# Kernel tuning notes

Hardware: AMD Instinct MI355X
Metric: run time of the kernel (lower is better)

The kernel has to match this reference:

```python
import jax, jax.numpy as jnp
import numpy as np

N = 20000
E = 320000
IN_C = 256
HID = 64
OUT_C = 64
NUM_LAYERS = 3
HEADS = 8


def setup_inputs() -> dict:
    key = jax.random.key(0)
    ks = jax.random.split(key, 12)
    s_in = 1.0 / np.sqrt(IN_C)
    s_h = 1.0 / np.sqrt(HID)
    inp = {
        "x": jax.random.normal(ks[0], (N, IN_C), dtype=jnp.float32),
        "edge_index": jax.random.randint(ks[1], (2, E), 0, N, dtype=jnp.int64),
        "lin1_w": jax.random.uniform(ks[2], (IN_C, HID), jnp.float32, -s_in, s_in),
        "lin1_b": jnp.zeros((HID,), jnp.float32),
        "wq": jax.random.uniform(ks[3], (NUM_LAYERS, HID, HID), jnp.float32, -s_h, s_h),
        "bq": jnp.zeros((NUM_LAYERS, HID), jnp.float32),
        "wk": jax.random.uniform(ks[4], (NUM_LAYERS, HID, HID), jnp.float32, -s_h, s_h),
        "bk": jnp.zeros((NUM_LAYERS, HID), jnp.float32),
        "wv": jax.random.uniform(ks[5], (NUM_LAYERS, HID, HID), jnp.float32, -s_h, s_h),
        "bv": jnp.zeros((NUM_LAYERS, HID), jnp.float32),
        "lin2_w": jax.random.uniform(ks[6], (HID, OUT_C), jnp.float32, -s_h, s_h),
        "lin2_b": jnp.zeros((OUT_C,), jnp.float32),
    }
    return inp


def reference(x, edge_index, lin1_w, lin1_b, wq, bq, wk, bk, wv, bv, lin2_w, lin2_b):
    n = x.shape[0]
    C = lin1_w.shape[1]
    d = C // HEADS  # per-head dim
    inv_sqrt_d = 1.0 / (d ** 0.5)

    # gcn_norm with self-loops (symmetric normalization, edge weights = 1)
    loop = jnp.arange(n, dtype=edge_index.dtype)
    row = jnp.concatenate([edge_index[0], loop])  # source j
    col = jnp.concatenate([edge_index[1], loop])  # target i
    deg = jax.ops.segment_sum(jnp.ones_like(col, dtype=x.dtype), col, num_segments=n)
    dinv = jnp.where(deg > 0, deg ** -0.5, 0.0)
    norm = dinv[row] * dinv[col]  # [E+N]

    # input projection (dropout inactive in eval mode)
    h = jax.nn.relu(x @ lin1_w + lin1_b)
    x_all = h[:, None, :]  # [N, 1, C] growing history

    for l in range(NUM_LAYERS):
        t = x_all.shape[1]
        # node-level projections (linear commutes with gather)
        q = x_all[:, -1] @ wq[l] + bq[l]                      # [N, C]
        k = jnp.einsum("ntc,cd->ntd", x_all, wk[l]) + bk[l]   # [N, t, C]
        v = jnp.einsum("ntc,cd->ntd", x_all, wv[l]) + bv[l]   # [N, t, C]
        # per-edge multi-head attention of target's latest repr over source history
        Qe = q[col].reshape(-1, HEADS, d)                      # [E', H, d]
        Ke = k[row].reshape(-1, t, HEADS, d)                   # [E', t, H, d]
        Ve = v[row].reshape(-1, t, HEADS, d)
        scores = jnp.einsum("ehd,ethd->eht", Qe, Ke) * inv_sqrt_d
        attn = jax.nn.softmax(scores, axis=-1)                 # [E', H, t]
        msg = jnp.einsum("eht,ethd->ehd", attn, Ve).reshape(-1, C)
        msg = msg * norm[:, None]
        out = jax.ops.segment_sum(msg, col, num_segments=n)    # sum aggregation
        out = jax.nn.relu(out)
        x_all = jnp.concatenate([x_all, out[:, None, :]], axis=1)

    logits = x_all[:, -1] @ lin2_w + lin2_b
    return jax.nn.log_softmax(logits, axis=1)
```

## Files before the change

### kernel.cpp

```cpp
#include <hip/hip_runtime.h>
#include <math.h>

#define HID 64
#define HEADS 8
#define NUM_LAYERS 3

typedef __attribute__((ext_vector_type(8))) short bf16x8;
typedef __attribute__((ext_vector_type(4))) float f32x4;

__device__ __forceinline__ unsigned short f2bf(float f) {
    union { float f; unsigned int u; } cv; cv.f = f;
    unsigned int u = cv.u;
    unsigned int r = (u + 0x7FFFu + ((u >> 16) & 1u)) >> 16;
    return (unsigned short)r;
}
__device__ __forceinline__ float bflo(unsigned int u) {
    union { unsigned int u; float f; } cv; cv.u = u << 16; return cv.f;
}
__device__ __forceinline__ float bfhi(unsigned int u) {
    union { unsigned int u; float f; } cv; cv.u = u & 0xFFFF0000u; return cv.f;
}
__device__ __forceinline__ unsigned relu_pk(unsigned u) {
    unsigned m = ((u & 0x8000u) ? 0u : 0xFFFFu) |
                 ((u & 0x80000000u) ? 0u : 0xFFFF0000u);
    return u & m;
}

__global__ void k_count(const int* __restrict__ col, int* __restrict__ counts, int E) {
    int e = blockIdx.x * blockDim.x + threadIdx.x;
    if (e < E) atomicAdd(&counts[col[e]], 1);
}

__global__ __launch_bounds__(1024) void k_scan(const int* __restrict__ counts,
                                               int* __restrict__ start,
                                               float* __restrict__ dinv, int n) {
    __shared__ int wsum[16];
    int tid = threadIdx.x;
    int lane = tid & 63, wv = tid >> 6;
    int ipt = (n + 1023) >> 10;
    int c0 = tid * ipt;
    int c1 = min(n, c0 + ipt);
    int s = 0;
    for (int i = c0; i < c1; ++i) s += counts[i];
    int x = s;
#pragma unroll
    for (int off = 1; off < 64; off <<= 1) {
        int y = __shfl_up(x, off);
        if (lane >= off) x += y;
    }
    if (lane == 63) wsum[wv] = x;
    __syncthreads();
    if (wv == 0 && lane < 16) {
        int t2 = wsum[lane];
#pragma unroll
        for (int off = 1; off < 16; off <<= 1) {
            int y = __shfl_up(t2, off);
            if (lane >= off) t2 += y;
        }
        wsum[lane] = t2;
    }
    __syncthreads();
    int waveoff = (wv > 0) ? wsum[wv - 1] : 0;
    int run = waveoff + x - s;
    for (int i = c0; i < c1; ++i) {
        int v = counts[i];
        start[i] = run;
        dinv[i] = rsqrtf((float)(v + 1));
        run += v;
    }
    if (tid == 0) start[n] = wsum[15];
}

__global__ void k_scatter(const int* __restrict__ ei, const int* __restrict__ start,
                          int* __restrict__ fill, int* __restrict__ ebuf, int E) {
    int e = blockIdx.x * blockDim.x + threadIdx.x;
    if (e >= E) return;
    int r = ei[e], c = ei[E + e];
    int pos = start[c] + atomicAdd(&fill[c], 1);
    ebuf[pos] = r;
}

#define ALD 72

__device__ __forceinline__ void stage_w_bf16(unsigned short* Wt,
                                             const float* __restrict__ w, int tid) {
    for (int idx = tid; idx < 1024; idx += 256) {
        int k = idx >> 4, n4 = (idx & 15) * 4;
        float4 wv = *(const float4*)&w[k * 64 + n4];
        Wt[(n4 + 0) * ALD + k] = f2bf(wv.x);
        Wt[(n4 + 1) * ALD + k] = f2bf(wv.y);
        Wt[(n4 + 2) * ALD + k] = f2bf(wv.z);
        Wt[(n4 + 3) * ALD + k] = f2bf(wv.w);
    }
}

__device__ __forceinline__ void mfma_step(const unsigned short* Alds,
                                          const unsigned short* Wt,
                                          int tid, f32x4 acc[4]) {
    int lane = tid & 63;
    int m0 = (tid >> 6) * 16;
    int c16 = lane & 15, quad = lane >> 4;
    const unsigned short* ar = &Alds[(m0 + c16) * ALD + quad * 8];
    bf16x8 a0 = *(const bf16x8*)ar;
    bf16x8 a1 = *(const bf16x8*)(ar + 32);
#pragma unroll
    for (int nt = 0; nt < 4; ++nt) {
        const unsigned short* br = &Wt[(nt * 16 + c16) * ALD + quad * 8];
        bf16x8 b0 = *(const bf16x8*)br;
        bf16x8 b1 = *(const bf16x8*)(br + 32);
        acc[nt] = __builtin_amdgcn_mfma_f32_16x16x32_bf16(a0, b0, acc[nt], 0, 0, 0);
        acc[nt] = __builtin_amdgcn_mfma_f32_16x16x32_bf16(a1, b1, acc[nt], 0, 0, 0);
    }
}

__global__ __launch_bounds__(256, 4) void k_lin1(
    const float* __restrict__ x, const float* __restrict__ w,
    const float* __restrict__ b, const float* __restrict__ wv0,
    const float* __restrict__ bv0, unsigned short* __restrict__ h,
    unsigned short* __restrict__ kv, int n) {
    __shared__ __align__(16) unsigned short Alds[64 * ALD];
    __shared__ __align__(16) unsigned short Wt[64 * ALD];
    int tid = threadIdx.x;
    int node0 = blockIdx.x * 64;
    f32x4 acc[4];
#pragma unroll
    for (int nt = 0; nt < 4; ++nt) acc[nt] = (f32x4){0.f, 0.f, 0.f, 0.f};

    for (int kc = 0; kc < 256; kc += 64) {
        __syncthreads();
        stage_w_bf16(Wt, w + kc * 64, tid);
        for (int idx = tid; idx < 1024; idx += 256) {
            int r = idx >> 4, c4 = (idx & 15) * 4;
            int node = node0 + r;
            float4 v = make_float4(0.f, 0.f, 0.f, 0.f);
            if (node < n) v = *(const float4*)&x[(size_t)node * 256 + kc + c4];
            Alds[r * ALD + c4 + 0] = f2bf(v.x);
            Alds[r * ALD + c4 + 1] = f2bf(v.y);
            Alds[r * ALD + c4 + 2] = f2bf(v.z);
            Alds[r * ALD + c4 + 3] = f2bf(v.w);
        }
        __syncthreads();
        mfma_step(Alds, Wt, tid, acc);
    }
    int lane = tid & 63;
    int m0 = (tid >> 6) * 16, c16 = lane & 15, quad = lane >> 4;
    float bias[4];
#pragma unroll
    for (int nt = 0; nt < 4; ++nt) bias[nt] = b[nt * 16 + c16];

    __syncthreads();
    stage_w_bf16(Wt, wv0, tid);
#pragma unroll
    for (int i = 0; i < 4; ++i) {
        int row = m0 + quad * 4 + i;
        int node = node0 + row;
#pragma unroll
        for (int nt = 0; nt < 4; ++nt) {
            unsigned short hb = f2bf(fmaxf(acc[nt][i] + bias[nt], 0.f));
            Alds[row * ALD + nt * 16 + c16] = hb;
            if (node < n) h[(size_t)node * 64 + nt * 16 + c16] = hb;
        }
    }
    __syncthreads();
    f32x4 acc2[4];
#pragma unroll
    for (int nt = 0; nt < 4; ++nt) acc2[nt] = (f32x4){0.f, 0.f, 0.f, 0.f};
    mfma_step(Alds, Wt, tid, acc2);
    float bias2[4];
#pragma unroll
    for (int nt = 0; nt < 4; ++nt) bias2[nt] = bv0[nt * 16 + c16];
#pragma unroll
    for (int i = 0; i < 4; ++i) {
        int node = node0 + m0 + quad * 4 + i;
        if (node < n) {
#pragma unroll
            for (int nt = 0; nt < 4; ++nt)
                kv[(size_t)node * 64 + nt * 16 + c16] = f2bf(acc2[nt][i] + bias2[nt]);
        }
    }
}

__global__ __launch_bounds__(256, 4) void k_qkv(
    const unsigned short* __restrict__ xsbase,
    const float* __restrict__ wq, const float* __restrict__ bq,
    const float* __restrict__ wk, const float* __restrict__ bk,
    const float* __restrict__ wv, const float* __restrict__ bv,
    float* __restrict__ q, unsigned short* __restrict__ kv,
    int n, int layer, int t, int kv_stride) {
    int job = blockIdx.y;
    const unsigned short* src; const float* w; const float* b; bool relu_in;
    int kv_off = 0;
    if (job == 0) {
        src = xsbase + (size_t)layer * n * 64;
        w = wq + layer * 4096; b = bq + layer * 64;
        relu_in = (layer >= 1);
    } else if (job <= t) {
        int s = job - 1;
        src = xsbase + (size_t)s * n * 64;
        w = wk + layer * 4096; b = bk + layer * 64;
        kv_off = s * 128;
        relu_in = (s >= 1);
    } else {
        int s = job - t - 1;
        src = xsbase + (size_t)s * n * 64;
        w = wv + layer * 4096; b = bv + layer * 64;
        kv_off = s * 128 + 64;
        relu_in = (s >= 1);
    }
    __shared__ __align__(16) unsigned short Alds[64 * ALD];
    __shared__ __align__(16) unsigned short Wt[64 * ALD];
    int tid = threadIdx.x;
    int node0 = blockIdx.x * 64;
    stage_w_bf16(Wt, w, tid);
    for (int idx = tid; idx < 512; idx += 256) {
        int r = idx >> 3, seg = idx & 7;
        int node = node0 + r;
        uint4 u = make_uint4(0u, 0u, 0u, 0u);
        if (node < n) u = *(const uint4*)&src[(size_t)node * 64 + seg * 8];
        if (relu_in) {
            u.x = relu_pk(u.x); u.y = relu_pk(u.y);
            u.z = relu_pk(u.z); u.w = relu_pk(u.w);
        }
        *(uint4*)&Alds[r * ALD + seg * 8] = u;
    }
    __syncthreads();
    f32x4 acc[4];
#pragma unroll
    for (int nt = 0; nt < 4; ++nt) acc[nt] = (f32x4){0.f, 0.f, 0.f, 0.f};
    mfma_step(Alds, Wt, tid, acc);

    int lane = tid & 63;
    int m0 = (tid >> 6) * 16, c16 = lane & 15, quad = lane >> 4;
    float bias[4];
#pragma unroll
    for (int nt = 0; nt < 4; ++nt) bias[nt] = b[nt * 16 + c16];
    if (job == 0) {
#pragma unroll
        for (int i = 0; i < 4; ++i) {
            int node = node0 + m0 + quad * 4 + i;
            if (node < n) {
#pragma unroll
                for (int nt = 0; nt < 4; ++nt)
                    q[(size_t)node * 64 + nt * 16 + c16] = acc[nt][i] + bias[nt];
            }
        }
    } else {
#pragma unroll
        for (int i = 0; i < 4; ++i) {
            int node = node0 + m0 + quad * 4 + i;
            if (node < n) {
#pragma unroll
                for (int nt = 0; nt < 4; ++nt)
                    kv[(size_t)node * kv_stride + kv_off + nt * 16 + c16] =
                        f2bf(acc[nt][i] + bias[nt]);
            }
        }
    }
}

template <int T>
__global__ __launch_bounds__(256) void k_attn_g(
    const int* __restrict__ start, const int* __restrict__ ebuf,
    const float* __restrict__ dinv, const float* __restrict__ q,
    const unsigned short* __restrict__ kv, unsigned short* __restrict__ outp, int n) {
    const int KVS = (T == 1) ? 64 : T * 128;
    int node = (int)((blockIdx.x * (size_t)blockDim.x + threadIdx.x) >> 6);
    int lane = threadIdx.x & 63;
    if (node >= n) return;
    int g = lane >> 3;
    int cb = (lane & 7) * 8;
    const float isd = 0.35355339059327373f;

    float qv[8];
    if (T > 1) {
        float4 q0 = *(const float4*)&q[(size_t)node * 64 + cb];
        float4 q1 = *(const float4*)&q[(size_t)node * 64 + cb + 4];
        qv[0] = q0.x; qv[1] = q0.y; qv[2] = q0.z; qv[3] = q0.w;
        qv[4] = q1.x; qv[5] = q1.y; qv[6] = q1.z; qv[7] = q1.w;
    }
    float dc = dinv[node];
    int s0 = start[node];
    int cnt = start[node + 1] - s0 + 1;

    float acc[8];
#pragma unroll
    for (int k = 0; k < 8; ++k) acc[k] = 0.f;

    for (int base = 0; base < cnt; base += 8) {
        int idx = base + g;
        bool valid = idx < cnt;
        int r = node;
        if (valid && idx > 0) r = ebuf[s0 + idx - 1];
        float dr = valid ? dinv[r] : 0.f;
        const unsigned short* rkv = kv + (size_t)r * KVS;

        float sc[T];
        float wgt;
        if (T > 1) {
            float m = -1e30f;
#pragma unroll
            for (int s = 0; s < T; ++s) {
                uint4 ku = *(const uint4*)&rkv[s * 128 + cb];
                float p = qv[0] * bflo(ku.x) + qv[1] * bfhi(ku.x)
                        + qv[2] * bflo(ku.y) + qv[3] * bfhi(ku.y)
                        + qv[4] * bflo(ku.z) + qv[5] * bfhi(ku.z)
                        + qv[6] * bflo(ku.w) + qv[7] * bfhi(ku.w);
                p *= isd;
                sc[s] = p;
                m = fmaxf(m, p);
            }
            float denom = 0.f;
#pragma unroll
            for (int s = 0; s < T; ++s) { sc[s] = __expf(sc[s] - m); denom += sc[s]; }
            wgt = dr / denom;
        } else {
            sc[0] = 1.f;
            wgt = dr;
        }

        float mg[8];
#pragma unroll
        for (int k = 0; k < 8; ++k) mg[k] = 0.f;
#pragma unroll
        for (int s = 0; s < T; ++s) {
            uint4 vu = *(const uint4*)&rkv[((T == 1) ? 0 : s * 128 + 64) + cb];
            float wv_ = sc[s];
            mg[0] += wv_ * bflo(vu.x); mg[1] += wv_ * bfhi(vu.x);
            mg[2] += wv_ * bflo(vu.y); mg[3] += wv_ * bfhi(vu.y);
            mg[4] += wv_ * bflo(vu.z); mg[5] += wv_ * bfhi(vu.z);
            mg[6] += wv_ * bflo(vu.w); mg[7] += wv_ * bfhi(vu.w);
        }
#pragma unroll
        for (int k = 0; k < 8; ++k) acc[k] += wgt * mg[k];
    }

#pragma unroll
    for (int off = 8; off < 64; off <<= 1) {
#pragma unroll
        for (int k = 0; k < 8; ++k) acc[k] += __shfl_xor(acc[k], off);
    }
    if (g == 0) {
        ushort4 o0, o1;
        o0.x = f2bf(acc[0] * dc); o0.y = f2bf(acc[1] * dc);
        o0.z = f2bf(acc[2] * dc); o0.w = f2bf(acc[3] * dc);
        o1.x = f2bf(acc[4] * dc); o1.y = f2bf(acc[5] * dc);
        o1.z = f2bf(acc[6] * dc); o1.w = f2bf(acc[7] * dc);
        *(ushort4*)&outp[(size_t)node * 64 + cb] = o0;
        *(ushort4*)&outp[(size_t)node * 64 + cb + 4] = o1;
    }
}

__global__ __launch_bounds__(256) void k_attn3f(
    const int* __restrict__ start, const int* __restrict__ ebuf,
    const float* __restrict__ dinv, const float* __restrict__ q,
    const unsigned short* __restrict__ kv,
    const float* __restrict__ w2, const float* __restrict__ b2,
    float* __restrict__ outp, int n) {
    const int T = 3, KVS = 384;
    int node = (int)((blockIdx.x * (size_t)blockDim.x + threadIdx.x) >> 6);
    int lane = threadIdx.x & 63;
    if (node >= n) return;
    int g = lane >> 3;
    int cb = (lane & 7) * 8;
    const float isd = 0.35355339059327373f;

    float qv[8];
    {
        float4 q0 = *(const float4*)&q[(size_t)node * 64 + cb];
        float4 q1 = *(const float4*)&q[(size_t)node * 64 + cb + 4];
        qv[0] = q0.x; qv[1] = q0.y; qv[2] = q0.z; qv[3] = q0.w;
        qv[4] = q1.x; qv[5] = q1.y; qv[6] = q1.z; qv[7] = q1.w;
    }
    float dc = dinv[node];
    int s0 = start[node];
    int cnt = start[node + 1] - s0 + 1;

    float acc[8];
#pragma unroll
    for (int k = 0; k < 8; ++k) acc[k] = 0.f;

    for (int base = 0; base < cnt; base += 8) {
        int idx = base + g;
        bool valid = idx < cnt;
        int r = node;
        if (valid && idx > 0) r = ebuf[s0 + idx - 1];
        float dr = valid ? dinv[r] : 0.f;
        const unsigned short* rkv = kv + (size_t)r * KVS;

        float sc[T];
        float m = -1e30f;
#pragma unroll
        for (int s = 0; s < T; ++s) {
            uint4 ku = *(const uint4*)&rkv[s * 128 + cb];
            float p = qv[0] * bflo(ku.x) + qv[1] * bfhi(ku.x)
                    + qv[2] * bflo(ku.y) + qv[3] * bfhi(ku.y)
                    + qv[4] * bflo(ku.z) + qv[5] * bfhi(ku.z)
                    + qv[6] * bflo(ku.w) + qv[7] * bfhi(ku.w);
            p *= isd;
            sc[s] = p;
            m = fmaxf(m, p);
        }
        float denom = 0.f;
#pragma unroll
        for (int s = 0; s < T; ++s) { sc[s] = __expf(sc[s] - m); denom += sc[s]; }
        float wgt = dr / denom;

        float mg[8];
#pragma unroll
        for (int k = 0; k < 8; ++k) mg[k] = 0.f;
#pragma unroll
        for (int s = 0; s < T; ++s) {
            uint4 vu = *(const uint4*)&rkv[s * 128 + 64 + cb];
            float wv_ = sc[s];
            mg[0] += wv_ * bflo(vu.x); mg[1] += wv_ * bfhi(vu.x);
            mg[2] += wv_ * bflo(vu.y); mg[3] += wv_ * bfhi(vu.y);
            mg[4] += wv_ * bflo(vu.z); mg[5] += wv_ * bfhi(vu.z);
            mg[6] += wv_ * bflo(vu.w); mg[7] += wv_ * bfhi(vu.w);
        }
#pragma unroll
        for (int k = 0; k < 8; ++k) acc[k] += wgt * mg[k];
    }

#pragma unroll
    for (int off = 8; off < 64; off <<= 1) {
#pragma unroll
        for (int k = 0; k < 8; ++k) acc[k] += __shfl_xor(acc[k], off);
    }
    float lg = b2[lane];
#pragma unroll
    for (int c = 0; c < 64; ++c) {
        float xc = fmaxf(__shfl(acc[c & 7], c >> 3) * dc, 0.f);
        lg += xc * w2[c * 64 + lane];
    }
    float mx = lg;
#pragma unroll
    for (int off = 1; off < 64; off <<= 1) mx = fmaxf(mx, __shfl_xor(mx, off));
    float e = __expf(lg - mx);
    float ssum = e;
#pragma unroll
    for (int off = 1; off < 64; off <<= 1) ssum += __shfl_xor(ssum, off);
    outp[(size_t)node * 64 + lane] = lg - mx - __logf(ssum);
}

extern "C" void kernel_launch(void* const* d_in, const int* in_sizes, int n_in,
                              void* d_out, int out_size, void* d_ws, size_t ws_size,
                              hipStream_t stream) {
    const float* x  = (const float*)d_in[0];
    const int*   ei = (const int*)d_in[1];
    const float* w1 = (const float*)d_in[2];
    const float* b1 = (const float*)d_in[3];
    const float* wq = (const float*)d_in[4];
    const float* bq = (const float*)d_in[5];
    const float* wk = (const float*)d_in[6];
    const float* bk = (const float*)d_in[7];
    const float* wv = (const float*)d_in[8];
    const float* bv = (const float*)d_in[9];
    const float* w2 = (const float*)d_in[10];
    const float* b2 = (const float*)d_in[11];
    float* outp = (float*)d_out;

    int n = in_sizes[0] / 256;
    int E = in_sizes[1] / 2;

    float* ws = (float*)d_ws;
    size_t off = 0;
    float* dinv = ws + off; off += (size_t)n;
    float* q    = ws + off; off += (size_t)n * 64;
    unsigned short* xsU = (unsigned short*)(ws + off); off += (size_t)n * 96;
    unsigned short* kvU = (unsigned short*)(ws + off); off += (size_t)n * 192;
    int* wsI    = (int*)(ws + off);
    int* counts = wsI;
    int* fill   = wsI + n;
    int* startA = wsI + 2 * n;
    int* ebuf   = wsI + 3 * n + 1;

    hipMemsetAsync(counts, 0, 2 * (size_t)n * sizeof(int), stream);
    k_count<<<(E + 255) / 256, 256, 0, stream>>>(ei + E, counts, E);
    k_scan<<<1, 1024, 0, stream>>>(counts, startA, dinv, n);
    k_scatter<<<(E + 255) / 256, 256, 0, stream>>>(ei, startA, fill, ebuf, E);

    k_lin1<<<(n + 63) / 64, 256, 0, stream>>>(x, w1, b1, wv, bv, xsU, kvU, n);

    int attn_grid = (int)(((size_t)n * 64 + 255) / 256);

    k_attn_g<1><<<attn_grid, 256, 0, stream>>>(startA, ebuf, dinv, q, kvU,
                                               xsU + (size_t)n * 64, n);
    {
        dim3 grid((n + 63) / 64, 5);
        k_qkv<<<grid, 256, 0, stream>>>(xsU, wq, bq, wk, bk, wv, bv,
                                        q, kvU, n, 1, 2, 256);
        k_attn_g<2><<<attn_grid, 256, 0, stream>>>(startA, ebuf, dinv, q, kvU,
                                                   xsU + (size_t)n * 128, n);
    }
    {
        dim3 grid((n + 63) / 64, 7);
        k_qkv<<<grid, 256, 0, stream>>>(xsU, wq, bq, wk, bk, wv, bv,
                                        q, kvU, n, 2, 3, 384);
        k_attn3f<<<attn_grid, 256, 0, stream>>>(startA, ebuf, dinv, q, kvU,
                                                w2, b2, outp, n);
    }
}
```

Before: 265.6 us.

## Fuse whole pipeline into one cooperative persistent kernel with grid syncs

Replaces the sequence of separate launches (memset, count, scan, scatter, lin1, three attention layers and qkv projections) with one cooperative persistent kernel that separates phases with grid.sync. It also overlaps independent work inside phases: the degree count runs alongside lin1, and the layer-1/2 K/V projections of the lin1 output run alongside the scan. KV buffers are split per layer so these projections can be computed early. The aim is to remove launch gaps and tail idle time, at the cost of grid-wide barriers, a single block doing the scan, and fewer resident waves for the attention phases; the old launch path is kept as a fallback if the cooperative launch fails.

```diff
diff --git a/kernel.cpp b/kernel.cpp
--- a/kernel.cpp
+++ b/kernel.cpp
@@ -1,9 +1,13 @@
 #include <hip/hip_runtime.h>
+#include <hip/hip_cooperative_groups.h>
 #include <math.h>
+
+namespace cg = cooperative_groups;
 
 #define HID 64
 #define HEADS 8
 #define NUM_LAYERS 3
+#define ALD 72
 
 typedef __attribute__((ext_vector_type(8))) short bf16x8;
 typedef __attribute__((ext_vector_type(4))) float f32x4;
@@ -25,62 +29,6 @@
                  ((u & 0x80000000u) ? 0u : 0xFFFF0000u);
     return u & m;
 }
-
-__global__ void k_count(const int* __restrict__ col, int* __restrict__ counts, int E) {
-    int e = blockIdx.x * blockDim.x + threadIdx.x;
-    if (e < E) atomicAdd(&counts[col[e]], 1);
-}
-
-__global__ __launch_bounds__(1024) void k_scan(const int* __restrict__ counts,
-                                               int* __restrict__ start,
-                                               float* __restrict__ dinv, int n) {
-    __shared__ int wsum[16];
-    int tid = threadIdx.x;
-    int lane = tid & 63, wv = tid >> 6;
-    int ipt = (n + 1023) >> 10;
-    int c0 = tid * ipt;
-    int c1 = min(n, c0 + ipt);
-    int s = 0;
-    for (int i = c0; i < c1; ++i) s += counts[i];
-    int x = s;
-#pragma unroll
-    for (int off = 1; off < 64; off <<= 1) {
-        int y = __shfl_up(x, off);
-        if (lane >= off) x += y;
-    }
-    if (lane == 63) wsum[wv] = x;
-    __syncthreads();
-    if (wv == 0 && lane < 16) {
-        int t2 = wsum[lane];
-#pragma unroll
-        for (int off = 1; off < 16; off <<= 1) {
-            int y = __shfl_up(t2, off);
-            if (lane >= off) t2 += y;
-        }
-        wsum[lane] = t2;
-    }
-    __syncthreads();
-    int waveoff = (wv > 0) ? wsum[wv - 1] : 0;
-    int run = waveoff + x - s;
-    for (int i = c0; i < c1; ++i) {
-        int v = counts[i];
-        start[i] = run;
-        dinv[i] = rsqrtf((float)(v + 1));
-        run += v;
-    }
-    if (tid == 0) start[n] = wsum[15];
-}
-
-__global__ void k_scatter(const int* __restrict__ ei, const int* __restrict__ start,
-                          int* __restrict__ fill, int* __restrict__ ebuf, int E) {
-    int e = blockIdx.x * blockDim.x + threadIdx.x;
-    if (e >= E) return;
-    int r = ei[e], c = ei[E + e];
-    int pos = start[c] + atomicAdd(&fill[c], 1);
-    ebuf[pos] = r;
-}
-
-#define ALD 72
 
 __device__ __forceinline__ void stage_w_bf16(unsigned short* Wt,
                                              const float* __restrict__ w, int tid) {
@@ -113,15 +61,64 @@
     }
 }
 
-__global__ __launch_bounds__(256, 4) void k_lin1(
+__device__ __forceinline__ void qkv_tile_body(
+    const unsigned short* __restrict__ src, const float* __restrict__ w,
+    const float* __restrict__ b, float* __restrict__ qd,
+    unsigned short* __restrict__ kvdst, int kv_stride, int kv_off, bool relu_in,
+    int node0, int n, int tid, unsigned short* Alds, unsigned short* Wt) {
+    stage_w_bf16(Wt, w, tid);
+    for (int idx = tid; idx < 512; idx += 256) {
+        int r = idx >> 3, seg = idx & 7;
+        int node = node0 + r;
+        uint4 u = make_uint4(0u, 0u, 0u, 0u);
+        if (node < n) u = *(const uint4*)&src[(size_t)node * 64 + seg * 8];
+        if (relu_in) {
+            u.x = relu_pk(u.x); u.y = relu_pk(u.y);
+            u.z = relu_pk(u.z); u.w = relu_pk(u.w);
+        }
+        *(uint4*)&Alds[r * ALD + seg * 8] = u;
+    }
+    __syncthreads();
+    f32x4 acc[4];
+#pragma unroll
+    for (int nt = 0; nt < 4; ++nt) acc[nt] = (f32x4){0.f, 0.f, 0.f, 0.f};
+    mfma_step(Alds, Wt, tid, acc);
+
+    int lane = tid & 63;
+    int m0 = (tid >> 6) * 16, c16 = lane & 15, quad = lane >> 4;
+    float bias[4];
+#pragma unroll
+    for (int nt = 0; nt < 4; ++nt) bias[nt] = b[nt * 16 + c16];
+    if (qd) {
+#pragma unroll
+        for (int i = 0; i < 4; ++i) {
+            int node = node0 + m0 + quad * 4 + i;
+            if (node < n) {
+#pragma unroll
+                for (int nt = 0; nt < 4; ++nt)
+                    qd[(size_t)node * 64 + nt * 16 + c16] = acc[nt][i] + bias[nt];
+            }
+        }
+    } else {
+#pragma unroll
+        for (int i = 0; i < 4; ++i) {
+            int node = node0 + m0 + quad * 4 + i;
+            if (node < n) {
+#pragma unroll
+                for (int nt = 0; nt < 4; ++nt)
+                    kvdst[(size_t)node * kv_stride + kv_off + nt * 16 + c16] =
+                        f2bf(acc[nt][i] + bias[nt]);
+            }
+        }
+    }
+}
+
+__device__ __forceinline__ void lin1_tile_body(
     const float* __restrict__ x, const float* __restrict__ w,
     const float* __restrict__ b, const float* __restrict__ wv0,
     const float* __restrict__ bv0, unsigned short* __restrict__ h,
-    unsigned short* __restrict__ kv, int n) {
-    __shared__ __align__(16) unsigned short Alds[64 * ALD];
-    __shared__ __align__(16) unsigned short Wt[64 * ALD];
-    int tid = threadIdx.x;
-    int node0 = blockIdx.x * 64;
+    unsigned short* __restrict__ kv, int n, int node0, int tid,
+    unsigned short* Alds, unsigned short* Wt) {
     f32x4 acc[4];
 #pragma unroll
     for (int nt = 0; nt < 4; ++nt) acc[nt] = (f32x4){0.f, 0.f, 0.f, 0.f};
@@ -180,6 +177,396 @@
     }
 }
 
+__device__ __forceinline__ void scan256_body(const int* __restrict__ counts,
+                                             int* __restrict__ start,
+                                             float* __restrict__ dinv, int n,
+                                             int tid, int* sscan) {
+    int lane = tid & 63, wvi = tid >> 6;
+    int ipt = (n + 255) >> 8;
+    int c0 = tid * ipt;
+    int c1 = min(n, c0 + ipt);
+    int s = 0;
+    for (int i = c0; i < c1; ++i) s += counts[i];
+    int x = s;
+#pragma unroll
+    for (int off = 1; off < 64; off <<= 1) {
+        int y = __shfl_up(x, off);
+        if (lane >= off) x += y;
+    }
+    if (lane == 63) sscan[wvi] = x;
+    __syncthreads();
+    if (tid == 0) {
+        int r = 0;
+#pragma unroll
+        for (int i = 0; i < 4; ++i) { int t = sscan[i]; sscan[i + 4] = r; r += t; }
+        start[n] = r;
+    }
+    __syncthreads();
+    int run = sscan[wvi + 4] + (x - s);
+    for (int i = c0; i < c1; ++i) {
+        int v = counts[i];
+        start[i] = run;
+        dinv[i] = rsqrtf((float)(v + 1));
+        run += v;
+    }
+}
+
+template <int T>
+__device__ __forceinline__ void attn_body(
+    int node, int lane, const int* __restrict__ start, const int* __restrict__ ebuf,
+    const float* __restrict__ dinv, const float* __restrict__ q,
+    const unsigned short* __restrict__ kv, unsigned short* __restrict__ outp) {
+    const int KVS = (T == 1) ? 64 : T * 128;
+    int g = lane >> 3;
+    int cb = (lane & 7) * 8;
+    const float isd = 0.35355339059327373f;
+
+    float qv[8];
+    if (T > 1) {
+        float4 q0 = *(const float4*)&q[(size_t)node * 64 + cb];
+        float4 q1 = *(const float4*)&q[(size_t)node * 64 + cb + 4];
+        qv[0] = q0.x; qv[1] = q0.y; qv[2] = q0.z; qv[3] = q0.w;
+        qv[4] = q1.x; qv[5] = q1.y; qv[6] = q1.z; qv[7] = q1.w;
+    }
+    float dc = dinv[node];
+    int s0 = start[node];
+    int cnt = start[node + 1] - s0 + 1;
+
+    float acc[8];
+#pragma unroll
+    for (int k = 0; k < 8; ++k) acc[k] = 0.f;
+
+    for (int base = 0; base < cnt; base += 8) {
+        int idx = base + g;
+        bool valid = idx < cnt;
+        int r = node;
+        if (valid && idx > 0) r = ebuf[s0 + idx - 1];
+        float dr = valid ? dinv[r] : 0.f;
+        const unsigned short* rkv = kv + (size_t)r * KVS;
+
+        float sc[T];
+        float wgt;
+        if (T > 1) {
+            float m = -1e30f;
+#pragma unroll
+            for (int s = 0; s < T; ++s) {
+                uint4 ku = *(const uint4*)&rkv[s * 128 + cb];
+                float p = qv[0] * bflo(ku.x) + qv[1] * bfhi(ku.x)
+                        + qv[2] * bflo(ku.y) + qv[3] * bfhi(ku.y)
+                        + qv[4] * bflo(ku.z) + qv[5] * bfhi(ku.z)
+                        + qv[6] * bflo(ku.w) + qv[7] * bfhi(ku.w);
+                p *= isd;
+                sc[s] = p;
+                m = fmaxf(m, p);
+            }
+            float denom = 0.f;
+#pragma unroll
+            for (int s = 0; s < T; ++s) { sc[s] = __expf(sc[s] - m); denom += sc[s]; }
+            wgt = dr / denom;
+        } else {
+            sc[0] = 1.f;
+            wgt = dr;
+        }
+
+        float mg[8];
+#pragma unroll
+        for (int k = 0; k < 8; ++k) mg[k] = 0.f;
+#pragma unroll
+        for (int s = 0; s < T; ++s) {
+            uint4 vu = *(const uint4*)&rkv[((T == 1) ? 0 : s * 128 + 64) + cb];
+            float wv_ = sc[s];
+            mg[0] += wv_ * bflo(vu.x); mg[1] += wv_ * bfhi(vu.x);
+            mg[2] += wv_ * bflo(vu.y); mg[3] += wv_ * bfhi(vu.y);
+            mg[4] += wv_ * bflo(vu.z); mg[5] += wv_ * bfhi(vu.z);
+            mg[6] += wv_ * bflo(vu.w); mg[7] += wv_ * bfhi(vu.w);
+        }
+#pragma unroll
+        for (int k = 0; k < 8; ++k) acc[k] += wgt * mg[k];
+    }
+
+#pragma unroll
+    for (int off = 8; off < 64; off <<= 1) {
+#pragma unroll
+        for (int k = 0; k < 8; ++k) acc[k] += __shfl_xor(acc[k], off);
+    }
+    if (g == 0) {
+        ushort4 o0, o1;
+        o0.x = f2bf(acc[0] * dc); o0.y = f2bf(acc[1] * dc);
+        o0.z = f2bf(acc[2] * dc); o0.w = f2bf(acc[3] * dc);
+        o1.x = f2bf(acc[4] * dc); o1.y = f2bf(acc[5] * dc);
+        o1.z = f2bf(acc[6] * dc); o1.w = f2bf(acc[7] * dc);
+        *(ushort4*)&outp[(size_t)node * 64 + cb] = o0;
+        *(ushort4*)&outp[(size_t)node * 64 + cb + 4] = o1;
+    }
+}
+
+__device__ __forceinline__ void attn3_body(
+    int node, int lane, const int* __restrict__ start, const int* __restrict__ ebuf,
+    const float* __restrict__ dinv, const float* __restrict__ q,
+    const unsigned short* __restrict__ kv, const float* __restrict__ w2,
+    const float* __restrict__ b2, float* __restrict__ outp) {
+    const int T = 3, KVS = 384;
+    int g = lane >> 3;
+    int cb = (lane & 7) * 8;
+    const float isd = 0.35355339059327373f;
+
+    float qv[8];
+    {
+        float4 q0 = *(const float4*)&q[(size_t)node * 64 + cb];
+        float4 q1 = *(const float4*)&q[(size_t)node * 64 + cb + 4];
+        qv[0] = q0.x; qv[1] = q0.y; qv[2] = q0.z; qv[3] = q0.w;
+        qv[4] = q1.x; qv[5] = q1.y; qv[6] = q1.z; qv[7] = q1.w;
+    }
+    float dc = dinv[node];
+    int s0 = start[node];
+    int cnt = start[node + 1] - s0 + 1;
+
+    float acc[8];
+#pragma unroll
+    for (int k = 0; k < 8; ++k) acc[k] = 0.f;
+
+    for (int base = 0; base < cnt; base += 8) {
+        int idx = base + g;
+        bool valid = idx < cnt;
+        int r = node;
+        if (valid && idx > 0) r = ebuf[s0 + idx - 1];
+        float dr = valid ? dinv[r] : 0.f;
+        const unsigned short* rkv = kv + (size_t)r * KVS;
+
+        float sc[T];
+        float m = -1e30f;
+#pragma unroll
+        for (int s = 0; s < T; ++s) {
+            uint4 ku = *(const uint4*)&rkv[s * 128 + cb];
+            float p = qv[0] * bflo(ku.x) + qv[1] * bfhi(ku.x)
+                    + qv[2] * bflo(ku.y) + qv[3] * bfhi(ku.y)
+                    + qv[4] * bflo(ku.z) + qv[5] * bfhi(ku.z)
+                    + qv[6] * bflo(ku.w) + qv[7] * bfhi(ku.w);
+            p *= isd;
+            sc[s] = p;
+            m = fmaxf(m, p);
+        }
+        float denom = 0.f;
+#pragma unroll
+        for (int s = 0; s < T; ++s) { sc[s] = __expf(sc[s] - m); denom += sc[s]; }
+        float wgt = dr / denom;
+
+        float mg[8];
+#pragma unroll
+        for (int k = 0; k < 8; ++k) mg[k] = 0.f;
+#pragma unroll
+        for (int s = 0; s < T; ++s) {
+            uint4 vu = *(const uint4*)&rkv[s * 128 + 64 + cb];
+            float wv_ = sc[s];
+            mg[0] += wv_ * bflo(vu.x); mg[1] += wv_ * bfhi(vu.x);
+            mg[2] += wv_ * bflo(vu.y); mg[3] += wv_ * bfhi(vu.y);
+            mg[4] += wv_ * bflo(vu.z); mg[5] += wv_ * bfhi(vu.z);
+            mg[6] += wv_ * bflo(vu.w); mg[7] += wv_ * bfhi(vu.w);
+        }
+#pragma unroll
+        for (int k = 0; k < 8; ++k) acc[k] += wgt * mg[k];
+    }
+
+#pragma unroll
+    for (int off = 8; off < 64; off <<= 1) {
+#pragma unroll
+        for (int k = 0; k < 8; ++k) acc[k] += __shfl_xor(acc[k], off);
+    }
+    float lg = b2[lane];
+#pragma unroll
+    for (int c = 0; c < 64; ++c) {
+        float xc = fmaxf(__shfl(acc[c & 7], c >> 3) * dc, 0.f);
+        lg += xc * w2[c * 64 + lane];
+    }
+    float mx = lg;
+#pragma unroll
+    for (int off = 1; off < 64; off <<= 1) mx = fmaxf(mx, __shfl_xor(mx, off));
+    float e = __expf(lg - mx);
+    float ssum = e;
+#pragma unroll
+    for (int off = 1; off < 64; off <<= 1) ssum += __shfl_xor(ssum, off);
+    outp[(size_t)node * 64 + lane] = lg - mx - __logf(ssum);
+}
+
+__global__ __launch_bounds__(256, 4) void k_mega(
+    const float* __restrict__ x, const int* __restrict__ ei,
+    const float* __restrict__ w1, const float* __restrict__ b1,
+    const float* __restrict__ wq, const float* __restrict__ bq,
+    const float* __restrict__ wk, const float* __restrict__ bk,
+    const float* __restrict__ wv, const float* __restrict__ bv,
+    const float* __restrict__ w2, const float* __restrict__ b2,
+    float* __restrict__ outp, float* __restrict__ dinv, float* __restrict__ qbuf,
+    unsigned short* __restrict__ xsU, unsigned short* __restrict__ kv0,
+    unsigned short* __restrict__ kv1, unsigned short* __restrict__ kv2,
+    int* __restrict__ counts, int* __restrict__ fill, int* __restrict__ startA,
+    int* __restrict__ ebuf, int n, int E) {
+    cg::grid_group grid = cg::this_grid();
+    __shared__ __align__(16) unsigned short Alds[64 * ALD];
+    __shared__ __align__(16) unsigned short Wt[64 * ALD];
+    __shared__ int sscan[8];
+    const int tid = threadIdx.x;
+    const int bid = blockIdx.x;
+    const int NB = gridDim.x;
+    const int NT = (n + 63) >> 6;
+    const int lane = tid & 63;
+    const int wid = (bid << 2) + (tid >> 6);
+    const int nw = NB << 2;
+
+    for (int i = bid * 256 + tid; i < n; i += NB * 256) counts[i] = 0;
+    for (int i = bid * 256 + tid; i < n; i += NB * 256) fill[i] = 0;
+    grid.sync();
+
+    {
+        int l1b = (NB * 3) >> 2;
+        int L1B = NT < l1b ? NT : l1b;
+        if (L1B < 1) L1B = 1;
+        if (bid < L1B) {
+            for (int t = bid; t < NT; t += L1B)
+                lin1_tile_body(x, w1, b1, wv, bv, xsU, kv0, n, t << 6, tid, Alds, Wt);
+        } else {
+            int cb = bid - L1B, ncb = NB - L1B;
+            for (int e = cb * 256 + tid; e < E; e += ncb * 256)
+                atomicAdd(&counts[ei[E + e]], 1);
+        }
+    }
+    grid.sync();
+
+    if (bid == 0) {
+        scan256_body(counts, startA, dinv, n, tid, sscan);
+    } else {
+        for (int t = bid - 1; t < 4 * NT; t += NB - 1) {
+            int job = t / NT, tile = t - job * NT;
+            const float* w; const float* b; unsigned short* dst; int stride, koff;
+            if (job == 0)      { w = wk + 4096; b = bk + 64;  dst = kv1; stride = 256; koff = 0;  }
+            else if (job == 1) { w = wv + 4096; b = bv + 64;  dst = kv1; stride = 256; koff = 64; }
+            else if (job == 2) { w = wk + 8192; b = bk + 128; dst = kv2; stride = 384; koff = 0;  }
+            else               { w = wv + 8192; b = bv + 128; dst = kv2; stride = 384; koff = 64; }
+            __syncthreads();
+            qkv_tile_body(xsU, w, b, nullptr, dst, stride, koff, false,
+                          tile << 6, n, tid, Alds, Wt);
+        }
+    }
+    grid.sync();
+
+    for (int e = bid * 256 + tid; e < E; e += NB * 256) {
+        int r = ei[e], c = ei[E + e];
+        int pos = startA[c] + atomicAdd(&fill[c], 1);
+        ebuf[pos] = r;
+    }
+    grid.sync();
+
+    for (int node = wid; node < n; node += nw)
+        attn_body<1>(node, lane, startA, ebuf, dinv, qbuf, kv0, xsU + (size_t)n * 64);
+    grid.sync();
+
+    {
+        const unsigned short* xs1 = xsU + (size_t)n * 64;
+        for (int t = bid; t < 5 * NT; t += NB) {
+            int job = t / NT, tile = t - job * NT;
+            const float* w; const float* b;
+            float* qd = nullptr; unsigned short* dst = nullptr;
+            int stride = 0, koff = 0;
+            if (job == 0)      { w = wq + 4096; b = bq + 64; qd = qbuf; }
+            else if (job == 1) { w = wk + 4096; b = bk + 64;  dst = kv1; stride = 256; koff = 128; }
+            else if (job == 2) { w = wv + 4096; b = bv + 64;  dst = kv1; stride = 256; koff = 192; }
+            else if (job == 3) { w = wk + 8192; b = bk + 128; dst = kv2; stride = 384; koff = 128; }
+            else               { w = wv + 8192; b = bv + 128; dst = kv2; stride = 384; koff = 192; }
+            __syncthreads();
+            qkv_tile_body(xs1, w, b, qd, dst, stride, koff, true,
+                          tile << 6, n, tid, Alds, Wt);
+        }
+    }
+    grid.sync();
+
+    for (int node = wid; node < n; node += nw)
+        attn_body<2>(node, lane, startA, ebuf, dinv, qbuf, kv1, xsU + (size_t)n * 128);
+    grid.sync();
+
+    {
+        const unsigned short* xs2 = xsU + (size_t)n * 128;
+        for (int t = bid; t < 3 * NT; t += NB) {
+            int job = t / NT, tile = t - job * NT;
+            const float* w; const float* b;
+            float* qd = nullptr; unsigned short* dst = nullptr;
+            int stride = 0, koff = 0;
+            if (job == 0)      { w = wq + 8192; b = bq + 128; qd = qbuf; }
+            else if (job == 1) { w = wk + 8192; b = bk + 128; dst = kv2; stride = 384; koff = 256; }
+            else               { w = wv + 8192; b = bv + 128; dst = kv2; stride = 384; koff = 320; }
+            __syncthreads();
+            qkv_tile_body(xs2, w, b, qd, dst, stride, koff, true,
+                          tile << 6, n, tid, Alds, Wt);
+        }
+    }
+    grid.sync();
+
+    for (int node = wid; node < n; node += nw)
+        attn3_body(node, lane, startA, ebuf, dinv, qbuf, kv2, w2, b2, outp);
+}
+
+__global__ void k_count(const int* __restrict__ col, int* __restrict__ counts, int E) {
+    int e = blockIdx.x * blockDim.x + threadIdx.x;
+    if (e < E) atomicAdd(&counts[col[e]], 1);
+}
+
+__global__ __launch_bounds__(1024) void k_scan(const int* __restrict__ counts,
+                                               int* __restrict__ start,
+                                               float* __restrict__ dinv, int n) {
+    __shared__ int wsum[16];
+    int tid = threadIdx.x;
+    int lane = tid & 63, wvi = tid >> 6;
+    int ipt = (n + 1023) >> 10;
+    int c0 = tid * ipt;
+    int c1 = min(n, c0 + ipt);
+    int s = 0;
+    for (int i = c0; i < c1; ++i) s += counts[i];
+    int x = s;
+#pragma unroll
+    for (int off = 1; off < 64; off <<= 1) {
+        int y = __shfl_up(x, off);
+        if (lane >= off) x += y;
+    }
+    if (lane == 63) wsum[wvi] = x;
+    __syncthreads();
+    if (wvi == 0 && lane < 16) {
+        int t2 = wsum[lane];
+#pragma unroll
+        for (int off = 1; off < 16; off <<= 1) {
+            int y = __shfl_up(t2, off);
+            if (lane >= off) t2 += y;
+        }
+        wsum[lane] = t2;
+    }
+    __syncthreads();
+    int waveoff = (wvi > 0) ? wsum[wvi - 1] : 0;
+    int run = waveoff + x - s;
+    for (int i = c0; i < c1; ++i) {
+        int v = counts[i];
+        start[i] = run;
+        dinv[i] = rsqrtf((float)(v + 1));
+        run += v;
+    }
+    if (tid == 0) start[n] = wsum[15];
+}
+
+__global__ void k_scatter(const int* __restrict__ ei, const int* __restrict__ start,
+                          int* __restrict__ fill, int* __restrict__ ebuf, int E) {
+    int e = blockIdx.x * blockDim.x + threadIdx.x;
+    if (e >= E) return;
+    int r = ei[e], c = ei[E + e];
+    int pos = start[c] + atomicAdd(&fill[c], 1);
+    ebuf[pos] = r;
+}
+
+__global__ __launch_bounds__(256, 4) void k_lin1(
+    const float* __restrict__ x, const float* __restrict__ w,
+    const float* __restrict__ b, const float* __restrict__ wv0,
+    const float* __restrict__ bv0, unsigned short* __restrict__ h,
+    unsigned short* __restrict__ kv, int n) {
+    __shared__ __align__(16) unsigned short Alds[64 * ALD];
+    __shared__ __align__(16) unsigned short Wt[64 * ALD];
+    lin1_tile_body(x, w, b, wv0, bv0, h, kv, n, blockIdx.x * 64, threadIdx.x, Alds, Wt);
+}
+
 __global__ __launch_bounds__(256, 4) void k_qkv(
     const unsigned short* __restrict__ xsbase,
     const float* __restrict__ wq, const float* __restrict__ bq,
@@ -189,11 +576,11 @@
     int n, int layer, int t, int kv_stride) {
     int job = blockIdx.y;
     const unsigned short* src; const float* w; const float* b; bool relu_in;
-    int kv_off = 0;
+    int kv_off = 0; float* qd = nullptr;
     if (job == 0) {
         src = xsbase + (size_t)layer * n * 64;
         w = wq + layer * 4096; b = bq + layer * 64;
-        relu_in = (layer >= 1);
+        relu_in = (layer >= 1); qd = q;
     } else if (job <= t) {
         int s = job - 1;
         src = xsbase + (size_t)s * n * 64;
@@ -209,53 +596,8 @@
     }
     __shared__ __align__(16) unsigned short Alds[64 * ALD];
     __shared__ __align__(16) unsigned short Wt[64 * ALD];
-    int tid = threadIdx.x;
-    int node0 = blockIdx.x * 64;
-    stage_w_bf16(Wt, w, tid);
-    for (int idx = tid; idx < 512; idx += 256) {
-        int r = idx >> 3, seg = idx & 7;
-        int node = node0 + r;
-        uint4 u = make_uint4(0u, 0u, 0u, 0u);
-        if (node < n) u = *(const uint4*)&src[(size_t)node * 64 + seg * 8];
-        if (relu_in) {
-            u.x = relu_pk(u.x); u.y = relu_pk(u.y);
-            u.z = relu_pk(u.z); u.w = relu_pk(u.w);
-        }
-        *(uint4*)&Alds[r * ALD + seg * 8] = u;
-    }
-    __syncthreads();
-    f32x4 acc[4];
-#pragma unroll
-    for (int nt = 0; nt < 4; ++nt) acc[nt] = (f32x4){0.f, 0.f, 0.f, 0.f};
-    mfma_step(Alds, Wt, tid, acc);
-
-    int lane = tid & 63;
-    int m0 = (tid >> 6) * 16, c16 = lane & 15, quad = lane >> 4;
-    float bias[4];
-#pragma unroll
-    for (int nt = 0; nt < 4; ++nt) bias[nt] = b[nt * 16 + c16];
-    if (job == 0) {
-#pragma unroll
-        for (int i = 0; i < 4; ++i) {
-            int node = node0 + m0 + quad * 4 + i;
-            if (node < n) {
-#pragma unroll
-                for (int nt = 0; nt < 4; ++nt)
-                    q[(size_t)node * 64 + nt * 16 + c16] = acc[nt][i] + bias[nt];
-            }
-        }
-    } else {
-#pragma unroll
-        for (int i = 0; i < 4; ++i) {
-            int node = node0 + m0 + quad * 4 + i;
-            if (node < n) {
-#pragma unroll
-                for (int nt = 0; nt < 4; ++nt)
-                    kv[(size_t)node * kv_stride + kv_off + nt * 16 + c16] =
-                        f2bf(acc[nt][i] + bias[nt]);
-            }
-        }
-    }
+    qkv_tile_body(src, w, b, qd, kv, kv_stride, kv_off, relu_in,
+                  blockIdx.x * 64, n, threadIdx.x, Alds, Wt);
 }
 
 template <int T>
@@ -263,91 +605,9 @@
     const int* __restrict__ start, const int* __restrict__ ebuf,
     const float* __restrict__ dinv, const float* __restrict__ q,
     const unsigned short* __restrict__ kv, unsigned short* __restrict__ outp, int n) {
-    const int KVS = (T == 1) ? 64 : T * 128;
     int node = (int)((blockIdx.x * (size_t)blockDim.x + threadIdx.x) >> 6);
-    int lane = threadIdx.x & 63;
     if (node >= n) return;
-    int g = lane >> 3;
-    int cb = (lane & 7) * 8;
-    const float isd = 0.35355339059327373f;
-
-    float qv[8];
-    if (T > 1) {
-        float4 q0 = *(const float4*)&q[(size_t)node * 64 + cb];
-        float4 q1 = *(const float4*)&q[(size_t)node * 64 + cb + 4];
-        qv[0] = q0.x; qv[1] = q0.y; qv[2] = q0.z; qv[3] = q0.w;
-        qv[4] = q1.x; qv[5] = q1.y; qv[6] = q1.z; qv[7] = q1.w;
-    }
-    float dc = dinv[node];
-    int s0 = start[node];
-    int cnt = start[node + 1] - s0 + 1;
-
-    float acc[8];
-#pragma unroll
-    for (int k = 0; k < 8; ++k) acc[k] = 0.f;
-
-    for (int base = 0; base < cnt; base += 8) {
-        int idx = base + g;
-        bool valid = idx < cnt;
-        int r = node;
-        if (valid && idx > 0) r = ebuf[s0 + idx - 1];
-        float dr = valid ? dinv[r] : 0.f;
-        const unsigned short* rkv = kv + (size_t)r * KVS;
-
-        float sc[T];
-        float wgt;
-        if (T > 1) {
-            float m = -1e30f;
-#pragma unroll
-            for (int s = 0; s < T; ++s) {
-                uint4 ku = *(const uint4*)&rkv[s * 128 + cb];
-                float p = qv[0] * bflo(ku.x) + qv[1] * bfhi(ku.x)
-                        + qv[2] * bflo(ku.y) + qv[3] * bfhi(ku.y)
-                        + qv[4] * bflo(ku.z) + qv[5] * bfhi(ku.z)
-                        + qv[6] * bflo(ku.w) + qv[7] * bfhi(ku.w);
-                p *= isd;
-                sc[s] = p;
-                m = fmaxf(m, p);
-            }
-            float denom = 0.f;
-#pragma unroll
-            for (int s = 0; s < T; ++s) { sc[s] = __expf(sc[s] - m); denom += sc[s]; }
-            wgt = dr / denom;
-        } else {
-            sc[0] = 1.f;
-            wgt = dr;
-        }
-
-        float mg[8];
-#pragma unroll
-        for (int k = 0; k < 8; ++k) mg[k] = 0.f;
-#pragma unroll
-        for (int s = 0; s < T; ++s) {
-            uint4 vu = *(const uint4*)&rkv[((T == 1) ? 0 : s * 128 + 64) + cb];
-            float wv_ = sc[s];
-            mg[0] += wv_ * bflo(vu.x); mg[1] += wv_ * bfhi(vu.x);
-            mg[2] += wv_ * bflo(vu.y); mg[3] += wv_ * bfhi(vu.y);
-            mg[4] += wv_ * bflo(vu.z); mg[5] += wv_ * bfhi(vu.z);
-            mg[6] += wv_ * bflo(vu.w); mg[7] += wv_ * bfhi(vu.w);
-        }
-#pragma unroll
-        for (int k = 0; k < 8; ++k) acc[k] += wgt * mg[k];
-    }
-
-#pragma unroll
-    for (int off = 8; off < 64; off <<= 1) {
-#pragma unroll
-        for (int k = 0; k < 8; ++k) acc[k] += __shfl_xor(acc[k], off);
-    }
-    if (g == 0) {
-        ushort4 o0, o1;
-        o0.x = f2bf(acc[0] * dc); o0.y = f2bf(acc[1] * dc);
-        o0.z = f2bf(acc[2] * dc); o0.w = f2bf(acc[3] * dc);
-        o1.x = f2bf(acc[4] * dc); o1.y = f2bf(acc[5] * dc);
-        o1.z = f2bf(acc[6] * dc); o1.w = f2bf(acc[7] * dc);
-        *(ushort4*)&outp[(size_t)node * 64 + cb] = o0;
-        *(ushort4*)&outp[(size_t)node * 64 + cb + 4] = o1;
-    }
+    attn_body<T>(node, threadIdx.x & 63, start, ebuf, dinv, q, kv, outp);
 }
 
 __global__ __launch_bounds__(256) void k_attn3f(
@@ -356,90 +616,9 @@
     const unsigned short* __restrict__ kv,
     const float* __restrict__ w2, const float* __restrict__ b2,
     float* __restrict__ outp, int n) {
-    const int T = 3, KVS = 384;
     int node = (int)((blockIdx.x * (size_t)blockDim.x + threadIdx.x) >> 6);
-    int lane = threadIdx.x & 63;
     if (node >= n) return;
-    int g = lane >> 3;
-    int cb = (lane & 7) * 8;
-    const float isd = 0.35355339059327373f;
-
-    float qv[8];
-    {
-        float4 q0 = *(const float4*)&q[(size_t)node * 64 + cb];
-        float4 q1 = *(const float4*)&q[(size_t)node * 64 + cb + 4];
-        qv[0] = q0.x; qv[1] = q0.y; qv[2] = q0.z; qv[3] = q0.w;
-        qv[4] = q1.x; qv[5] = q1.y; qv[6] = q1.z; qv[7] = q1.w;
-    }
-    float dc = dinv[node];
-    int s0 = start[node];
-    int cnt = start[node + 1] - s0 + 1;
-
-    float acc[8];
-#pragma unroll
-    for (int k = 0; k < 8; ++k) acc[k] = 0.f;
-
-    for (int base = 0; base < cnt; base += 8) {
-        int idx = base + g;
-        bool valid = idx < cnt;
-        int r = node;
-        if (valid && idx > 0) r = ebuf[s0 + idx - 1];
-        float dr = valid ? dinv[r] : 0.f;
-        const unsigned short* rkv = kv + (size_t)r * KVS;
-
-        float sc[T];
-        float m = -1e30f;
-#pragma unroll
-        for (int s = 0; s < T; ++s) {
-            uint4 ku = *(const uint4*)&rkv[s * 128 + cb];
-            float p = qv[0] * bflo(ku.x) + qv[1] * bfhi(ku.x)
-                    + qv[2] * bflo(ku.y) + qv[3] * bfhi(ku.y)
-                    + qv[4] * bflo(ku.z) + qv[5] * bfhi(ku.z)
-                    + qv[6] * bflo(ku.w) + qv[7] * bfhi(ku.w);
-            p *= isd;
-            sc[s] = p;
-            m = fmaxf(m, p);
-        }
-        float denom = 0.f;
-#pragma unroll
-        for (int s = 0; s < T; ++s) { sc[s] = __expf(sc[s] - m); denom += sc[s]; }
-        float wgt = dr / denom;
-
-        float mg[8];
-#pragma unroll
-        for (int k = 0; k < 8; ++k) mg[k] = 0.f;
-#pragma unroll
-        for (int s = 0; s < T; ++s) {
-            uint4 vu = *(const uint4*)&rkv[s * 128 + 64 + cb];
-            float wv_ = sc[s];
-            mg[0] += wv_ * bflo(vu.x); mg[1] += wv_ * bfhi(vu.x);
-            mg[2] += wv_ * bflo(vu.y); mg[3] += wv_ * bfhi(vu.y);
-            mg[4] += wv_ * bflo(vu.z); mg[5] += wv_ * bfhi(vu.z);
-            mg[6] += wv_ * bflo(vu.w); mg[7] += wv_ * bfhi(vu.w);
-        }
-#pragma unroll
-        for (int k = 0; k < 8; ++k) acc[k] += wgt * mg[k];
-    }
-
-#pragma unroll
-    for (int off = 8; off < 64; off <<= 1) {
-#pragma unroll
-        for (int k = 0; k < 8; ++k) acc[k] += __shfl_xor(acc[k], off);
-    }
-    float lg = b2[lane];
-#pragma unroll
-    for (int c = 0; c < 64; ++c) {
-        float xc = fmaxf(__shfl(acc[c & 7], c >> 3) * dc, 0.f);
-        lg += xc * w2[c * 64 + lane];
-    }
-    float mx = lg;
-#pragma unroll
-    for (int off = 1; off < 64; off <<= 1) mx = fmaxf(mx, __shfl_xor(mx, off));
-    float e = __expf(lg - mx);
-    float ssum = e;
-#pragma unroll
-    for (int off = 1; off < 64; off <<= 1) ssum += __shfl_xor(ssum, off);
-    outp[(size_t)node * 64 + lane] = lg - mx - __logf(ssum);
+    attn3_body(node, threadIdx.x & 63, start, ebuf, dinv, q, kv, w2, b2, outp);
 }
 
 extern "C" void kernel_launch(void* const* d_in, const int* in_sizes, int n_in,
@@ -467,36 +646,67 @@
     float* dinv = ws + off; off += (size_t)n;
     float* q    = ws + off; off += (size_t)n * 64;
     unsigned short* xsU = (unsigned short*)(ws + off); off += (size_t)n * 96;
-    unsigned short* kvU = (unsigned short*)(ws + off); off += (size_t)n * 192;
+    unsigned short* kv0 = (unsigned short*)(ws + off); off += (size_t)n * 32;
+    unsigned short* kv1 = (unsigned short*)(ws + off); off += (size_t)n * 128;
+    unsigned short* kv2 = (unsigned short*)(ws + off); off += (size_t)n * 192;
     int* wsI    = (int*)(ws + off);
     int* counts = wsI;
     int* fill   = wsI + n;
     int* startA = wsI + 2 * n;
     int* ebuf   = wsI + 3 * n + 1;
 
+    static int NB = -1;
+    if (NB < 0) {
+        int dev = 0;
+        (void)hipGetDevice(&dev);
+        int nCU = 0;
+        if (hipDeviceGetAttribute(&nCU, hipDeviceAttributeMultiprocessorCount, dev)
+                != hipSuccess || nCU <= 0)
+            nCU = 256;
+        int perCU = 0;
+        if (hipOccupancyMaxActiveBlocksPerMultiprocessor(
+                &perCU, reinterpret_cast<const void*>(k_mega), 256, 0) != hipSuccess ||
+            perCU < 1)
+            perCU = 1;
+        NB = nCU * perCU;
+        if (NB > 2048) NB = 2048;
+        if (NB < 64) NB = 64;
+    }
+
+    void* kargs[] = {
+        (void*)&x, (void*)&ei, (void*)&w1, (void*)&b1, (void*)&wq, (void*)&bq,
+        (void*)&wk, (void*)&bk, (void*)&wv, (void*)&bv, (void*)&w2, (void*)&b2,
+        (void*)&outp, (void*)&dinv, (void*)&q, (void*)&xsU, (void*)&kv0,
+        (void*)&kv1, (void*)&kv2, (void*)&counts, (void*)&fill, (void*)&startA,
+        (void*)&ebuf, (void*)&n, (void*)&E};
+    hipError_t err = hipLaunchCooperativeKernel(
+        reinterpret_cast<const void*>(k_mega), dim3(NB), dim3(256), kargs, 0, stream);
+    if (err == hipSuccess) return;
+    (void)hipGetLastError();
+
     hipMemsetAsync(counts, 0, 2 * (size_t)n * sizeof(int), stream);
     k_count<<<(E + 255) / 256, 256, 0, stream>>>(ei + E, counts, E);
     k_scan<<<1, 1024, 0, stream>>>(counts, startA, dinv, n);
     k_scatter<<<(E + 255) / 256, 256, 0, stream>>>(ei, startA, fill, ebuf, E);
 
-    k_lin1<<<(n + 63) / 64, 256, 0, stream>>>(x, w1, b1, wv, bv, xsU, kvU, n);
+    k_lin1<<<(n + 63) / 64, 256, 0, stream>>>(x, w1, b1, wv, bv, xsU, kv0, n);
 
     int attn_grid = (int)(((size_t)n * 64 + 255) / 256);
 
-    k_attn_g<1><<<attn_grid, 256, 0, stream>>>(startA, ebuf, dinv, q, kvU,
+    k_attn_g<1><<<attn_grid, 256, 0, stream>>>(startA, ebuf, dinv, q, kv0,
                                                xsU + (size_t)n * 64, n);
     {
         dim3 grid((n + 63) / 64, 5);
         k_qkv<<<grid, 256, 0, stream>>>(xsU, wq, bq, wk, bk, wv, bv,
-                                        q, kvU, n, 1, 2, 256);
-        k_attn_g<2><<<attn_grid, 256, 0, stream>>>(startA, ebuf, dinv, q, kvU,
+                                        q, kv1, n, 1, 2, 256);
+        k_attn_g<2><<<attn_grid, 256, 0, stream>>>(startA, ebuf, dinv, q, kv1,
                                                    xsU + (size_t)n * 128, n);
     }
     {
         dim3 grid((n + 63) / 64, 7);
         k_qkv<<<grid, 256, 0, stream>>>(xsU, wq, bq, wk, bk, wv, bv,
-                                        q, kvU, n, 2, 3, 384);
-        k_attn3f<<<attn_grid, 256, 0, stream>>>(startA, ebuf, dinv, q, kvU,
+                                        q, kv2, n, 2, 3, 384);
+        k_attn3f<<<attn_grid, 256, 0, stream>>>(startA, ebuf, dinv, q, kv2,
                                                 w2, b2, outp, n);
     }
 }
```

After: 845.2 us. 3.18x slower.
